# Kernel optimization log

Measured on AMD Instinct MI355X. Metric: run time of the kernel, lower is better.

The kernel has to match this reference:

```python
import jax, jax.numpy as jnp
import numpy as np
from jax import lax

FILTERS = 32
NEIGH = 5


def _conv3d_same(x, w, b=None):
    out = lax.conv_general_dilated(x, w, window_strides=(1, 1, 1), padding='SAME',
                                   dimension_numbers=('NCDHW', 'OIDHW', 'NCDHW'))
    return out if b is None else out + b[None, :, None, None, None]


def _avgpool2(x):
    s = lax.reduce_window(x, 0.0, lax.add, (1, 1, 2, 2, 2), (1, 1, 2, 2, 2), 'VALID')
    return s * 0.125


def _grid_sample_3d(vol, grid):
    # trilinear, zeros padding, align_corners=False (torch defaults)
    Din, Hin, Win = vol.shape
    ix = ((grid[..., 0] + 1.0) * Win - 1.0) * 0.5
    iy = ((grid[..., 1] + 1.0) * Hin - 1.0) * 0.5
    iz = ((grid[..., 2] + 1.0) * Din - 1.0) * 0.5
    x0f, y0f, z0f = jnp.floor(ix), jnp.floor(iy), jnp.floor(iz)
    wx, wy, wz = ix - x0f, iy - y0f, iz - z0f
    x0 = x0f.astype(jnp.int32); y0 = y0f.astype(jnp.int32); z0 = z0f.astype(jnp.int32)

    def tap(z, y, x, w):
        valid = (z >= 0) & (z < Din) & (y >= 0) & (y < Hin) & (x >= 0) & (x < Win)
        v = vol[jnp.clip(z, 0, Din - 1), jnp.clip(y, 0, Hin - 1), jnp.clip(x, 0, Win - 1)]
        return jnp.where(valid, v, 0.0) * w

    return (tap(z0,     y0,     x0,     (1 - wz) * (1 - wy) * (1 - wx))
          + tap(z0,     y0,     x0 + 1, (1 - wz) * (1 - wy) * wx)
          + tap(z0,     y0 + 1, x0,     (1 - wz) * wy * (1 - wx))
          + tap(z0,     y0 + 1, x0 + 1, (1 - wz) * wy * wx)
          + tap(z0 + 1, y0,     x0,     wz * (1 - wy) * (1 - wx))
          + tap(z0 + 1, y0,     x0 + 1, wz * (1 - wy) * wx)
          + tap(z0 + 1, y0 + 1, x0,     wz * wy * (1 - wx))
          + tap(z0 + 1, y0 + 1, x0 + 1, wz * wy * wx))


def _forward(x, conv_w, conv_b, gaus_w):
    D = _avgpool2(_conv3d_same(x, conv_w, conv_b))           # (B, c, h, w, d)
    p = _conv3d_same(D, gaus_w)                              # (B, c, h, w, d)
    B, c, h, w, d = D.shape
    # normalized coordinate field P: (3, h, w, d)
    P = jnp.stack([
        jnp.broadcast_to(jnp.arange(h, dtype=D.dtype)[:, None, None] / (h - 1), (h, w, d)),
        jnp.broadcast_to(jnp.arange(w, dtype=D.dtype)[None, :, None] / (w - 1), (h, w, d)),
        jnp.broadcast_to(jnp.arange(d, dtype=D.dtype)[None, None, :] / (d - 1), (h, w, d)),
    ])
    # (B, 3, c, h, w, d) -> (3B, c, h, w, d) for a single batched gaussian conv
    D_mul = (P[None, :, None] * D[:, None]).reshape(3 * B, c, h, w, d)
    allf = _conv3d_same(D_mul, gaus_w).reshape(B, 3, c, h, w, d)
    filt = jnp.clip(allf / (p[:, None] + 1e-6) * 2.0 - 1.0, -1.0, 1.0)
    grids = jnp.transpose(filt, (0, 2, 3, 4, 5, 1))          # (B, c, h, w, d, 3)
    Bx, Cx, Hx, Wx, Dx = x.shape
    vols = x.reshape(B * c, Hx, Wx, Dx)
    g = grids.reshape(B * c, h, w, d, 3)
    y = jax.vmap(_grid_sample_3d)(vols, g).reshape(B, c, h, w, d)
    return y, D, jnp.mean(grids, axis=1)


def setup_inputs() -> dict:
    key = jax.random.key(0)
    k1, k2, k3 = jax.random.split(key, 3)
    x = jax.random.normal(k1, (2, FILTERS, 64, 64, 64), dtype=jnp.float32)
    fan_in = FILTERS * 3 * 3 * 3
    conv_w = (jax.random.normal(k2, (FILTERS, FILTERS, 3, 3, 3), dtype=jnp.float32)
              / np.float32(np.sqrt(fan_in)))
    conv_b = jax.random.normal(k3, (FILTERS,), dtype=jnp.float32) * 0.01
    # fixed gaussian kernel, replicated across in/out channels (as in makegaussian)
    center = NEIGH // 2
    co = np.arange(NEIGH) - center
    zz, yy, xx = np.meshgrid(co, co, co, indexing='ij')
    gk = np.exp(-4.0 * np.log(2.0) * (zz ** 2 + yy ** 2 + xx ** 2) / NEIGH ** 2).astype(np.float32)
    gaus_w = jnp.asarray(np.broadcast_to(gk, (FILTERS, FILTERS, NEIGH, NEIGH, NEIGH)).copy())
    return {"x": x, "conv_w": conv_w, "conv_b": conv_b, "gaus_w": gaus_w}


def reference(x, conv_w, conv_b, gaus_w):
    return _forward(x, conv_w, conv_b, gaus_w)
```

## Files before the change

### kernel.cpp

```cpp
#include <hip/hip_runtime.h>
#include <hip/hip_bf16.h>


#define XN 64
#define DN 32
#define C  32
#define XVOL (XN * XN * XN)
#define DVOL (DN * DN * DN)

typedef __attribute__((ext_vector_type(8))) short short8v;
typedef __attribute__((ext_vector_type(4))) float float4v;

struct __attribute__((packed, aligned(4))) f4u { float4v v; };
struct __attribute__((packed, aligned(4))) s8u { short8v v; };

static __device__ __forceinline__ short f2bf(float f) {
    union { float f; unsigned u; } v; v.f = f;
    unsigned r = (v.u + 0x7fffu + ((v.u >> 16) & 1u)) >> 16;
    return (short)r;
}

static __device__ __forceinline__ unsigned pk2(float a, float b) {
    __hip_bfloat162 h = __float22bfloat162_rn(float2{a, b});
    union { __hip_bfloat162 h2; unsigned u; } cv; cv.h2 = h;
    return cv.u;
}

static __device__ __forceinline__ float4v shmask(float4v ld, float c, float l, float r) {
    float4v o;
    o[0] = fmaf(r, ld[1], c * ld[0]);
    o[1] = fmaf(l, ld[0], fmaf(r, ld[2], c * ld[1]));
    o[2] = fmaf(l, ld[1], fmaf(r, ld[3], c * ld[2]));
    o[3] = fmaf(l, ld[2], c * ld[3]);
    return o;
}

static __device__ __forceinline__ float w4val(const float* __restrict__ conv_w,
                                              int ic, int u, int oc) {
    int uz = u >> 4, uy = (u >> 2) & 3, ux = u & 3;
    float s = 0.f;
    #pragma unroll
    for (int sz = 0; sz < 2; ++sz) {
        int tz = uz - sz; if (tz < 0 || tz > 2) continue;
        #pragma unroll
        for (int sy = 0; sy < 2; ++sy) {
            int ty = uy - sy; if (ty < 0 || ty > 2) continue;
            #pragma unroll
            for (int sx = 0; sx < 2; ++sx) {
                int tx = ux - sx; if (tx < 0 || tx > 2) continue;
                s += conv_w[(oc * C + ic) * 27 + tz * 9 + ty * 3 + tx];
            }
        }
    }
    return 0.125f * s;
}

__global__ __launch_bounds__(256) void k_prep(const float* __restrict__ conv_w,
                                              const float* __restrict__ conv_b,
                                              unsigned short* __restrict__ wfrag,
                                              float* __restrict__ wsum) {
    int bid = blockIdx.x;
    int tid = threadIdx.x;
    if (bid < 256) {
        int i = bid * 256 + tid;
        int e = i & 7;
        int l = (i >> 3) & 63;
        int sf = i >> 9;
        int f = sf & 1, step = sf >> 1;
        int oc = f * 16 + (l & 15);
        int k = step * 32 + ((l >> 4) * 8 + e);
        float v = w4val(conv_w, k >> 6, k & 63, oc);
        wfrag[i] = (unsigned short)f2bf(v);
        if (i == 0) {
            float s = 0.f;
            for (int o = 0; o < C; ++o) s += conv_b[o];
            wsum[2048] = s;
        }
    } else {
        int i2 = (bid - 256) * 256 + tid;
        int oc = tid & 31;
        int kk = i2 >> 5;
        float v = w4val(conv_w, kk >> 6, kk & 63, oc);
        v += __shfl_xor(v, 1, 64);
        v += __shfl_xor(v, 2, 64);
        v += __shfl_xor(v, 4, 64);
        v += __shfl_xor(v, 8, 64);
        v += __shfl_xor(v, 16, 64);
        if (oc == 0) wsum[kk] = v;
    }
}

__global__ __launch_bounds__(256) void k_conv_mfma(
        const float* __restrict__ x, const unsigned short* __restrict__ wfrag,
        const float* __restrict__ wsum, const float* __restrict__ bias,
        float* __restrict__ Dout, float* __restrict__ Dsum) {
    __shared__ float wsl[2112];
    __shared__ char wbuf[2 * 8320];
    int tid = threadIdx.x;
    for (int i = tid; i < 513; i += 256)
        *(float4v*)&wsl[i * 4] = *(const float4v*)&wsum[i * 4];

    int bid = blockIdx.x;
    int wid = (bid & 7) * 128 + (bid >> 3);
    int xt = wid & 1;
    int yt = (wid >> 1) & 15;
    int zt = (wid >> 5) & 15;
    int b  = wid >> 9;
    int w = tid >> 6, lane = tid & 63;
    int col = lane & 15, g = lane >> 4;
    int pz = zt * 2 + (w >> 1), py = yt * 2 + (w & 1), px = xt * 16 + col;

    const char* xb = (const char*)(x + (size_t)b * C * XVOL);
    const char* wfb = (const char*)wfrag;

    int sdst = (tid >> 6) * 1040 + (tid & 63) * 16;

    int gxb = 2 * px - 1;
    int gxc = min(max(gxb, 0), XN - 4);
    int s = gxc - gxb;
    int offb[4];
    float mc[4], ml[4], mr[4];
    #pragma unroll
    for (int h = 0; h < 2; ++h)
    #pragma unroll
    for (int rs = 0; rs < 2; ++rs) {
        int gz = 2 * pz - 1 + 2 * h + (g >> 1);
        int gy = 2 * py - 1 + (g & 1) * 2 + rs;
        bool rv = (unsigned)gz < (unsigned)XN && (unsigned)gy < (unsigned)XN;
        int gzc = min(max(gz, 0), XN - 1);
        int gyc = min(max(gy, 0), XN - 1);
        int idx = h * 2 + rs;
        offb[idx] = ((gzc * XN + gyc) * XN + gxc) * 4;
        mc[idx] = (rv && s == 0)  ? 1.f : 0.f;
        ml[idx] = (rv && s == 1)  ? 1.f : 0.f;
        mr[idx] = (rv && s == -1) ? 1.f : 0.f;
    }

    float4v acc0 = {0.f, 0.f, 0.f, 0.f};
    float4v acc1 = {0.f, 0.f, 0.f, 0.f};
    float4v dpv = {0.f, 0.f, 0.f, 0.f};
    float4v tA[4], tB[4];
    short8v sg0, sg1;

#define LOADT(T, j) do {                                                     \
    const char* xp = xb + (size_t)(j) * (XVOL * 4);                          \
    _Pragma("unroll")                                                        \
    for (int i5 = 0; i5 < 4; ++i5)                                           \
        T[i5] = ((const f4u*)(xp + offb[i5]))->v;                            \
} while (0)

#define STAGE_LOAD(st) do {                                                  \
    const char* wp = wfb + (size_t)(st) * 8192 + tid * 16;                   \
    sg0 = ((const s8u*)(wp))->v;                                             \
    sg1 = ((const s8u*)(wp + 4096))->v;                                      \
} while (0)

#define STAGE_WRITE(bf) do {                                                 \
    *(short8v*)(wbuf + (bf) * 8320 + sdst) = sg0;                            \
    *(short8v*)(wbuf + (bf) * 8320 + 4160 + sdst) = sg1;                     \
} while (0)

#define COMPT(T, bf, icL, j) do {                                            \
    _Pragma("unroll")                                                        \
    for (int h5 = 0; h5 < 2; ++h5) {                                         \
        float4v r0 = shmask(T[h5 * 2],     mc[h5 * 2],     ml[h5 * 2],     mr[h5 * 2]);     \
        float4v r1 = shmask(T[h5 * 2 + 1], mc[h5 * 2 + 1], ml[h5 * 2 + 1], mr[h5 * 2 + 1]); \
        const float4v wlo = *(const float4v*)&wsl[((j) * 2 + h5) * 32 + g * 8];     \
        const float4v whi = *(const float4v*)&wsl[((j) * 2 + h5) * 32 + g * 8 + 4]; \
        dpv += wlo * r0;                                                     \
        dpv += whi * r1;                                                     \
        union { short8v s; unsigned u[4]; } Bv;                              \
        Bv.u[0] = pk2(r0[0], r0[1]); Bv.u[1] = pk2(r0[2], r0[3]);            \
        Bv.u[2] = pk2(r1[0], r1[1]); Bv.u[3] = pk2(r1[2], r1[3]);            \
        const char* wl = wbuf + (bf) * 8320 + (icL) * 4160 + lane * 16;      \
        short8v w0 = *(const short8v*)(wl + (h5 * 2) * 1040);                \
        short8v w1 = *(const short8v*)(wl + (h5 * 2 + 1) * 1040);            \
        acc0 = __builtin_amdgcn_mfma_f32_16x16x32_bf16(w0, Bv.s, acc0, 0, 0, 0); \
        acc1 = __builtin_amdgcn_mfma_f32_16x16x32_bf16(w1, Bv.s, acc1, 0, 0, 0); \
    }                                                                        \
} while (0)

    STAGE_LOAD(0);
    STAGE_WRITE(0);
    LOADT(tA, 0);
    LOADT(tB, 1);
    __syncthreads();

    for (int st = 0; st < 16; ++st) {
        int cur = st & 1;
        if (st < 15) STAGE_LOAD(st + 1);
        int ic = st * 2;
        COMPT(tA, cur, 0, ic);
        if (ic + 2 < C) LOADT(tA, ic + 2);
        COMPT(tB, cur, 1, ic + 1);
        if (ic + 3 < C) LOADT(tB, ic + 3);
        if (st < 15) {
            STAGE_WRITE(cur ^ 1);
            __syncthreads();
        }
    }

#undef LOADT
#undef STAGE_LOAD
#undef STAGE_WRITE
#undef COMPT

    float dp = (dpv[0] + dpv[1]) + (dpv[2] + dpv[3]);
    dp += __shfl_xor(dp, 16, 64);
    dp += __shfl_xor(dp, 32, 64);

    int sp = pz * (DN * DN) + py * DN + px;
    float4v b0 = *(const float4v*)&bias[g * 4];
    float4v b1 = *(const float4v*)&bias[16 + g * 4];
    #pragma unroll
    for (int r = 0; r < 4; ++r) {
        int oc0 = g * 4 + r;
        int oc1 = 16 + g * 4 + r;
        Dout[(size_t)(b * C + oc0) * DVOL + sp] = acc0[r] + b0[r];
        Dout[(size_t)(b * C + oc1) * DVOL + sp] = acc1[r] + b1[r];
    }
    if (g == 0)
        Dsum[b * DVOL + sp] = dp + wsl[2048];
}

__global__ __launch_bounds__(256) void k_gauss(const float* __restrict__ Dsum,
                                               const float* __restrict__ gaus_w,
                                               float* __restrict__ filt,
                                               float* __restrict__ outg) {
    __shared__ float tg[8 * 12 * 12];
    __shared__ float gk[125];
    int bid = blockIdx.x;
    int xt = bid & 3, yt = (bid >> 2) & 3, zt = (bid >> 4) & 7, b = bid >> 7;
    int tid = threadIdx.x;
    if (tid < 125) gk[tid] = gaus_w[tid];
    const float* Ds = Dsum + b * DVOL;
    for (int i = tid; i < 1152; i += 256) {
        int lx = i % 12; int r = i / 12; int ly = r % 12; int lz = r / 12;
        int gz = zt * 4 - 2 + lz, gy = yt * 8 - 2 + ly, gx = xt * 8 - 2 + lx;
        float v = 0.f;
        if ((unsigned)gz < DN && (unsigned)gy < DN && (unsigned)gx < DN)
            v = Ds[(gz * DN + gy) * DN + gx];
        tg[i] = v;
    }
    __syncthreads();
    int px = tid & 7, py = (tid >> 3) & 7, pz = tid >> 6;
    const float inv31 = 1.f / 31.f;
    float zb = (float)(zt * 4 + pz - 2);
    float yb = (float)(yt * 8 + py - 2);
    float xb = (float)(xt * 8 + px - 2);
    float p = 0.f, a0 = 0.f, a1 = 0.f, a2 = 0.f;
    for (int tz = 0; tz < 5; ++tz)
    for (int ty = 0; ty < 5; ++ty) {
        int base = ((pz + tz) * 12 + py + ty) * 12 + px;
        #pragma unroll
        for (int tx = 0; tx < 5; ++tx) {
            float g = gk[tz * 25 + ty * 5 + tx];
            float v = g * tg[base + tx];
            p += v;
            a0 = fmaf(v, (zb + (float)tz) * inv31, a0);
            a1 = fmaf(v, (yb + (float)ty) * inv31, a1);
            a2 = fmaf(v, (xb + (float)tx) * inv31, a2);
        }
    }
    float denom = p + 1e-6f;
    float f0 = fminf(fmaxf(a0 / denom * 2.f - 1.f, -1.f), 1.f);
    float f1 = fminf(fmaxf(a1 / denom * 2.f - 1.f, -1.f), 1.f);
    float f2 = fminf(fmaxf(a2 / denom * 2.f - 1.f, -1.f), 1.f);
    int sp = ((zt * 4 + pz) * DN + yt * 8 + py) * DN + xt * 8 + px;
    filt[(b * 3 + 0) * DVOL + sp] = f0;
    filt[(b * 3 + 1) * DVOL + sp] = f1;
    filt[(b * 3 + 2) * DVOL + sp] = f2;
    outg[(size_t)(b * DVOL + sp) * 3 + 0] = f0;
    outg[(size_t)(b * DVOL + sp) * 3 + 1] = f1;
    outg[(size_t)(b * DVOL + sp) * 3 + 2] = f2;
}

__global__ __launch_bounds__(128) void k_sample(const float* __restrict__ x,
                                                const float* __restrict__ filt,
                                                float* __restrict__ y) {
    int bid = blockIdx.x;
    int wid = (bid & 7) * 1024 + (bid >> 3);
    int xt = wid & 1;
    int yt = (wid >> 1) & 7;
    int zt = (wid >> 4) & 15;
    int cgrp = (wid >> 8) & 15;
    int b  = wid >> 12;
    int tid = threadIdx.x;
    int px = tid & 15, py = (tid >> 4) & 3, pz = tid >> 6;
    int sp = ((zt * 2 + pz) * DN + yt * 4 + py) * DN + xt * 16 + px;
    const float* fb = filt + b * 3 * DVOL;
    float g0 = fb[sp], g1 = fb[DVOL + sp], g2 = fb[2 * DVOL + sp];

    float ix = ((g0 + 1.0f) * (float)XN - 1.0f) * 0.5f;
    float iy = ((g1 + 1.0f) * (float)XN - 1.0f) * 0.5f;
    float iz = ((g2 + 1.0f) * (float)XN - 1.0f) * 0.5f;
    float x0f = floorf(ix), y0f = floorf(iy), z0f = floorf(iz);
    float wx = ix - x0f, wyf = iy - y0f, wz = iz - z0f;
    int x0 = (int)x0f, y0i = (int)y0f, z0 = (int)z0f;

    int offs[8];
    float wts[8];
    #pragma unroll
    for (int t = 0; t < 8; ++t) {
        int dz = t >> 2, dy = (t >> 1) & 1, dx = t & 1;
        int zc = z0 + dz, yc = y0i + dy, xc = x0 + dx;
        bool valid = (unsigned)zc < (unsigned)XN && (unsigned)yc < (unsigned)XN &&
                     (unsigned)xc < (unsigned)XN;
        int zcl = min(max(zc, 0), XN - 1);
        int ycl = min(max(yc, 0), XN - 1);
        int xcl = min(max(xc, 0), XN - 1);
        offs[t] = zcl * (XN * XN) + ycl * XN + xcl;
        float w = (dz ? wz : 1.f - wz) * (dy ? wyf : 1.f - wyf) * (dx ? wx : 1.f - wx);
        wts[t] = valid ? w : 0.f;
    }

    const float* xc0 = x + (size_t)(b * C + cgrp * 2) * XVOL;
    float t0[8], t1[8];
    #pragma unroll
    for (int k = 0; k < 8; ++k) t0[k] = xc0[offs[k]];
    #pragma unroll
    for (int k = 0; k < 8; ++k) t1[k] = xc0[XVOL + offs[k]];

    float a0 = 0.f, a1 = 0.f;
    #pragma unroll
    for (int k = 0; k < 8; ++k) a0 = fmaf(wts[k], t0[k], a0);
    #pragma unroll
    for (int k = 0; k < 8; ++k) a1 = fmaf(wts[k], t1[k], a1);
    y[(size_t)(b * C + cgrp * 2 + 0) * DVOL + sp] = a0;
    y[(size_t)(b * C + cgrp * 2 + 1) * DVOL + sp] = a1;
}

extern "C" void kernel_launch(void* const* d_in, const int* in_sizes, int n_in,
                              void* d_out, int out_size, void* d_ws, size_t ws_size,
                              hipStream_t stream) {
    const float* x      = (const float*)d_in[0];
    const float* conv_w = (const float*)d_in[1];
    const float* conv_b = (const float*)d_in[2];
    const float* gaus_w = (const float*)d_in[3];

    float* out = (float*)d_out;
    float* y_out = out;
    float* D_out = out + (size_t)2097152;
    float* g_out = out + (size_t)4194304;

    float* ws   = (float*)d_ws;
    float* Dsum = ws;
    float* filt = ws + 65536;
    float* wsum = ws + 262144;
    unsigned short* wfrag = (unsigned short*)(ws + 264256);

    k_prep<<<dim3(512), dim3(256), 0, stream>>>(conv_w, conv_b, wfrag, wsum);
    k_conv_mfma<<<dim3(1024), dim3(256), 0, stream>>>(x, wfrag, wsum, conv_b,
                                                      D_out, Dsum);
    k_gauss<<<dim3(256), dim3(256), 0, stream>>>(Dsum, gaus_w, filt, g_out);
    k_sample<<<dim3(8192), dim3(128), 0, stream>>>(x, filt, y_out);
    (void)in_sizes; (void)n_in; (void)out_size; (void)ws_size;
}
```

Baseline: 87.58 us.

## Stage input halo tile in shared memory instead of per-lane overlapping global loads

The conv kernel now cooperatively loads a 6x6x34 halo tile of each input channel into double-buffered LDS with boundary zeroing, then reads the MFMA operands from LDS. This replaces per-lane unaligned float4 global loads and the shift/mask arithmetic, and it removes redundant overlapping global reads. In exchange it adds an extra barrier per channel, scalar global loads and LDS traffic, and the pipeline ordering becomes more intricate.

```diff
diff --git a/kernel.cpp b/kernel.cpp
--- a/kernel.cpp
+++ b/kernel.cpp
@@ -24,15 +24,6 @@
     __hip_bfloat162 h = __float22bfloat162_rn(float2{a, b});
     union { __hip_bfloat162 h2; unsigned u; } cv; cv.h2 = h;
     return cv.u;
-}
-
-static __device__ __forceinline__ float4v shmask(float4v ld, float c, float l, float r) {
-    float4v o;
-    o[0] = fmaf(r, ld[1], c * ld[0]);
-    o[1] = fmaf(l, ld[0], fmaf(r, ld[2], c * ld[1]));
-    o[2] = fmaf(l, ld[1], fmaf(r, ld[3], c * ld[2]));
-    o[3] = fmaf(l, ld[2], c * ld[3]);
-    return o;
 }
 
 static __device__ __forceinline__ float w4val(const float* __restrict__ conv_w,
@@ -90,12 +81,16 @@
     }
 }
 
+#define NSTG (6 * 6 * 34)
+#define TILEF (6 * 6 * 36)
+
 __global__ __launch_bounds__(256) void k_conv_mfma(
         const float* __restrict__ x, const unsigned short* __restrict__ wfrag,
         const float* __restrict__ wsum, const float* __restrict__ bias,
         float* __restrict__ Dout, float* __restrict__ Dsum) {
     __shared__ float wsl[2112];
     __shared__ char wbuf[2 * 8320];
+    __shared__ float tile[2][TILEF];
     int tid = threadIdx.x;
     for (int i = tid; i < 513; i += 256)
         *(float4v*)&wsl[i * 4] = *(const float4v*)&wsum[i * 4];
@@ -108,71 +103,80 @@
     int b  = wid >> 9;
     int w = tid >> 6, lane = tid & 63;
     int col = lane & 15, g = lane >> 4;
-    int pz = zt * 2 + (w >> 1), py = yt * 2 + (w & 1), px = xt * 16 + col;
-
-    const char* xb = (const char*)(x + (size_t)b * C * XVOL);
+    int wpz = w >> 1, wpy = w & 1;
+    int pz = zt * 2 + wpz, py = yt * 2 + wpy, px = xt * 16 + col;
+
+    const float* xb = x + (size_t)b * C * XVOL;
     const char* wfb = (const char*)wfrag;
-
-    int sdst = (tid >> 6) * 1040 + (tid & 63) * 16;
-
-    int gxb = 2 * px - 1;
-    int gxc = min(max(gxb, 0), XN - 4);
-    int s = gxc - gxb;
-    int offb[4];
-    float mc[4], ml[4], mr[4];
-    #pragma unroll
-    for (int h = 0; h < 2; ++h)
-    #pragma unroll
-    for (int rs = 0; rs < 2; ++rs) {
-        int gz = 2 * pz - 1 + 2 * h + (g >> 1);
-        int gy = 2 * py - 1 + (g & 1) * 2 + rs;
-        bool rv = (unsigned)gz < (unsigned)XN && (unsigned)gy < (unsigned)XN;
-        int gzc = min(max(gz, 0), XN - 1);
-        int gyc = min(max(gy, 0), XN - 1);
-        int idx = h * 2 + rs;
-        offb[idx] = ((gzc * XN + gyc) * XN + gxc) * 4;
-        mc[idx] = (rv && s == 0)  ? 1.f : 0.f;
-        ml[idx] = (rv && s == 1)  ? 1.f : 0.f;
-        mr[idx] = (rv && s == -1) ? 1.f : 0.f;
-    }
+    int wsdst = (tid >> 6) * 1040 + (tid & 63) * 16;
+
+    int gz0 = zt * 4 - 1, gy0 = yt * 4 - 1, gx0 = xt * 32 - 1;
+    int  soff[5], sdst[5];
+    bool sval[5], swr[5];
+    #pragma unroll
+    for (int it = 0; it < 5; ++it) {
+        int i = tid + it * 256;
+        int lx = i % 34; int r = i / 34; int ly = r % 6; int lz = r / 6;
+        int gz = gz0 + lz, gy = gy0 + ly, gx = gx0 + lx;
+        bool inr = i < NSTG;
+        swr[it]  = inr;
+        sval[it] = inr && (unsigned)gz < XN && (unsigned)gy < XN && (unsigned)gx < XN;
+        soff[it] = ((gz & 63) * XN + (gy & 63)) * XN + (gx & 63);
+        sdst[it] = inr ? (lz * 6 + ly) * 36 + lx : 0;
+    }
+
+    int base_g = ((2 * wpz + (g >> 1)) * 6 + 2 * wpy + (g & 1) * 2) * 36 + 2 * col;
 
     float4v acc0 = {0.f, 0.f, 0.f, 0.f};
     float4v acc1 = {0.f, 0.f, 0.f, 0.f};
     float4v dpv = {0.f, 0.f, 0.f, 0.f};
-    float4v tA[4], tB[4];
+    float svA[5], svB[5];
     short8v sg0, sg1;
 
-#define LOADT(T, j) do {                                                     \
-    const char* xp = xb + (size_t)(j) * (XVOL * 4);                          \
+#define TLOAD(SV, j) do {                                                    \
+    const float* xp = xb + (size_t)(j) * XVOL;                               \
     _Pragma("unroll")                                                        \
-    for (int i5 = 0; i5 < 4; ++i5)                                           \
-        T[i5] = ((const f4u*)(xp + offb[i5]))->v;                            \
-} while (0)
-
-#define STAGE_LOAD(st) do {                                                  \
+    for (int it = 0; it < 5; ++it)                                           \
+        SV[it] = sval[it] ? xp[soff[it]] : 0.f;                              \
+} while (0)
+
+#define TWRITE(dst, SV) do {                                                 \
+    _Pragma("unroll")                                                        \
+    for (int it = 0; it < 5; ++it)                                           \
+        if (swr[it]) (dst)[sdst[it]] = SV[it];                               \
+} while (0)
+
+#define WLOAD(st) do {                                                       \
     const char* wp = wfb + (size_t)(st) * 8192 + tid * 16;                   \
     sg0 = ((const s8u*)(wp))->v;                                             \
     sg1 = ((const s8u*)(wp + 4096))->v;                                      \
 } while (0)
 
-#define STAGE_WRITE(bf) do {                                                 \
-    *(short8v*)(wbuf + (bf) * 8320 + sdst) = sg0;                            \
-    *(short8v*)(wbuf + (bf) * 8320 + 4160 + sdst) = sg1;                     \
-} while (0)
-
-#define COMPT(T, bf, icL, j) do {                                            \
+#define WWRITE(bf) do {                                                      \
+    *(short8v*)(wbuf + (bf) * 8320 + wsdst) = sg0;                           \
+    *(short8v*)(wbuf + (bf) * 8320 + 4160 + wsdst) = sg1;                    \
+} while (0)
+
+#define COMPT(ic) do {                                                       \
+    const float* t = tile[(ic) & 1];                                         \
     _Pragma("unroll")                                                        \
     for (int h5 = 0; h5 < 2; ++h5) {                                         \
-        float4v r0 = shmask(T[h5 * 2],     mc[h5 * 2],     ml[h5 * 2],     mr[h5 * 2]);     \
-        float4v r1 = shmask(T[h5 * 2 + 1], mc[h5 * 2 + 1], ml[h5 * 2 + 1], mr[h5 * 2 + 1]); \
-        const float4v wlo = *(const float4v*)&wsl[((j) * 2 + h5) * 32 + g * 8];     \
-        const float4v whi = *(const float4v*)&wsl[((j) * 2 + h5) * 32 + g * 8 + 4]; \
+        int off0 = base_g + h5 * 432;                                        \
+        float2 v01 = *(const float2*)&t[off0];                               \
+        float2 v23 = *(const float2*)&t[off0 + 2];                           \
+        float2 v45 = *(const float2*)&t[off0 + 36];                          \
+        float2 v67 = *(const float2*)&t[off0 + 38];                          \
+        float4v r0 = {v01.x, v01.y, v23.x, v23.y};                           \
+        float4v r1 = {v45.x, v45.y, v67.x, v67.y};                           \
+        const float4v wlo = *(const float4v*)&wsl[((ic) * 2 + h5) * 32 + g * 8];     \
+        const float4v whi = *(const float4v*)&wsl[((ic) * 2 + h5) * 32 + g * 8 + 4]; \
         dpv += wlo * r0;                                                     \
         dpv += whi * r1;                                                     \
         union { short8v s; unsigned u[4]; } Bv;                              \
         Bv.u[0] = pk2(r0[0], r0[1]); Bv.u[1] = pk2(r0[2], r0[3]);            \
         Bv.u[2] = pk2(r1[0], r1[1]); Bv.u[3] = pk2(r1[2], r1[3]);            \
-        const char* wl = wbuf + (bf) * 8320 + (icL) * 4160 + lane * 16;      \
+        const char* wl = wbuf + (((ic) >> 1) & 1) * 8320 + ((ic) & 1) * 4160 \
+                         + lane * 16;                                        \
         short8v w0 = *(const short8v*)(wl + (h5 * 2) * 1040);                \
         short8v w1 = *(const short8v*)(wl + (h5 * 2 + 1) * 1040);            \
         acc0 = __builtin_amdgcn_mfma_f32_16x16x32_bf16(w0, Bv.s, acc0, 0, 0, 0); \
@@ -180,29 +184,34 @@
     }                                                                        \
 } while (0)
 
-    STAGE_LOAD(0);
-    STAGE_WRITE(0);
-    LOADT(tA, 0);
-    LOADT(tB, 1);
+    WLOAD(0);
+    WWRITE(0);
+    {
+        float sv[5];
+        TLOAD(sv, 0);
+        TWRITE(tile[0], sv);
+    }
+    TLOAD(svB, 1);
     __syncthreads();
 
     for (int st = 0; st < 16; ++st) {
-        int cur = st & 1;
-        if (st < 15) STAGE_LOAD(st + 1);
-        int ic = st * 2;
-        COMPT(tA, cur, 0, ic);
-        if (ic + 2 < C) LOADT(tA, ic + 2);
-        COMPT(tB, cur, 1, ic + 1);
-        if (ic + 3 < C) LOADT(tB, ic + 3);
-        if (st < 15) {
-            STAGE_WRITE(cur ^ 1);
-            __syncthreads();
-        }
-    }
-
-#undef LOADT
-#undef STAGE_LOAD
-#undef STAGE_WRITE
+        int ic0 = 2 * st, ic1 = 2 * st + 1;
+        if (st > 0) __syncthreads();
+        TWRITE(tile[1], svB);
+        if (ic0 + 2 < C) TLOAD(svA, ic0 + 2);
+        if (st < 15) WLOAD(st + 1);
+        COMPT(ic0);
+        __syncthreads();
+        if (ic0 + 2 < C) TWRITE(tile[0], svA);
+        if (ic1 + 2 < C) TLOAD(svB, ic1 + 2);
+        COMPT(ic1);
+        if (st < 15) WWRITE((st + 1) & 1);
+    }
+
+#undef TLOAD
+#undef TWRITE
+#undef WLOAD
+#undef WWRITE
 #undef COMPT
 
     float dp = (dpv[0] + dpv[1]) + (dpv[2] + dpv[3]);
```

After: 84.51 us (median of 2 runs). 3.5% less time.
